# Kernel optimization log

Hardware: AMD Instinct MI355X
Metric: run time of the kernel (lower is better)

Reference implementation:

```python
import jax, jax.numpy as jnp
import numpy as np

B, C, S, HID = 64, 512, 28, 256  # batch, channels, spatial size, LSTM hidden


def _param(k, shape):
    return jax.random.normal(k, shape, jnp.float32) * 0.05


def setup_inputs() -> dict:
    key = jax.random.key(0)
    ks = jax.random.split(key, 19)
    inp = {"x": jax.random.normal(ks[0], (B, C, S, S), jnp.float32)}
    # vertical bidirectional LSTM (input C, hidden HID), torch gate order i,f,g,o
    inp["v_wih_f"] = _param(ks[1], (4 * HID, C))
    inp["v_whh_f"] = _param(ks[2], (4 * HID, HID))
    inp["v_b_f"] = _param(ks[3], (4 * HID,))
    inp["v_wih_b"] = _param(ks[4], (4 * HID, C))
    inp["v_whh_b"] = _param(ks[5], (4 * HID, HID))
    inp["v_b_b"] = _param(ks[6], (4 * HID,))
    # horizontal bidirectional LSTM (input 2*HID=512, hidden HID)
    inp["h_wih_f"] = _param(ks[7], (4 * HID, 2 * HID))
    inp["h_whh_f"] = _param(ks[8], (4 * HID, HID))
    inp["h_b_f"] = _param(ks[9], (4 * HID,))
    inp["h_wih_b"] = _param(ks[10], (4 * HID, 2 * HID))
    inp["h_whh_b"] = _param(ks[11], (4 * HID, HID))
    inp["h_b_b"] = _param(ks[12], (4 * HID,))
    # 1x1 conv 512 -> 100 (10x10 attention kernel logits)
    inp["conv_w"] = _param(ks[13], (100, 2 * HID))
    inp["conv_b"] = _param(ks[14], (100,))
    return inp


def _lstm_scan(xs, wih, whh, b):
    # xs: [T, N, D] -> h sequence [T, N, HID]
    hdim = whh.shape[1]
    def step(carry, xt):
        h, c = carry
        gates = xt @ wih.T + h @ whh.T + b  # [N, 4H]
        i, f, g, o = jnp.split(gates, 4, axis=-1)
        c = jax.nn.sigmoid(f) * c + jax.nn.sigmoid(i) * jnp.tanh(g)
        h = jax.nn.sigmoid(o) * jnp.tanh(c)
        return (h, c), h
    n = xs.shape[1]
    z = jnp.zeros((n, hdim), xs.dtype)
    _, hs = jax.lax.scan(step, (z, z), xs)
    return hs


def _bilstm(x, wf, uf, bf, wb, ub, bb):
    # x: [N, T, D] -> [N, T, 2*HID]
    xs = jnp.swapaxes(x, 0, 1)
    hf = _lstm_scan(xs, wf, uf, bf)
    hb = _lstm_scan(xs[::-1], wb, ub, bb)[::-1]
    return jnp.swapaxes(jnp.concatenate([hf, hb], axis=-1), 0, 1)


def reference(x, v_wih_f, v_whh_f, v_b_f, v_wih_b, v_whh_b, v_b_b,
              h_wih_f, h_whh_f, h_b_f, h_wih_b, h_whh_b, h_b_b,
              conv_w, conv_b):
    b, c, s, _ = x.shape
    xt = jnp.transpose(x, (0, 3, 2, 1))            # [B, W, H, C]
    # vertical LSTM: seq over W, batched over (B, H)
    v_in = jnp.transpose(xt, (0, 2, 1, 3)).reshape(b * s, s, c)
    v_out = _bilstm(v_in, v_wih_f, v_whh_f, v_b_f, v_wih_b, v_whh_b, v_b_b)
    v_out = jnp.transpose(v_out.reshape(b, s, s, 2 * HID), (0, 2, 1, 3))  # [B, W, H, 512]
    # horizontal LSTM: seq over H, batched over (B, W)
    h_in = v_out.reshape(b * s, s, 2 * HID)
    h_out = _bilstm(h_in, h_wih_f, h_whh_f, h_b_f, h_wih_b, h_whh_b, h_b_b)
    feat = jnp.transpose(h_out.reshape(b, s, s, 2 * HID), (0, 3, 2, 1))  # [B, 512, H, W]
    # 1x1 conv -> [B, 100, H, W], softmax over 100 kernel entries
    kern = jnp.einsum('bfhw,of->bohw', feat, conv_w) + conv_b[None, :, None, None]
    kern = jax.nn.softmax(kern, axis=1)
    # faithful to torch: C-order reshape [B,100,H,W] -> (B*H*W, 100) kernels
    w = kern.reshape(b, s * s, 100)
    # grouped dilated conv3d == weighted sum over dilation-3 sampled 10x10 grid
    x_s = x[:, :, ::3, ::3].reshape(b, c, 100)     # [B, C, 100]
    out = jnp.einsum('bpk,bck->bpc', w, x_s)       # [B, H*W, C]
    return out.reshape(b, c, s, s)                 # faithful C-order reshape
```

## Files before the change

### kernel.cpp

```cpp
#include <hip/hip_runtime.h>
#include <hip/hip_bf16.h>
#include <stdint.h>

typedef __hip_bfloat16 bf16_t;
typedef __attribute__((ext_vector_type(8))) short short8;
typedef __attribute__((ext_vector_type(4))) short short4v;
typedef __attribute__((ext_vector_type(4))) float f32x4;
typedef __attribute__((ext_vector_type(4))) unsigned int u32x4;
typedef unsigned long long ull;

#define MFMA16(a, b, c) __builtin_amdgcn_mfma_f32_16x16x32_bf16(a, b, c, 0, 0, 0)

#define NROW 50176
#define NBATCH 1792

__device__ __forceinline__ void g2l16(const void* g, void* l) {
  __builtin_amdgcn_global_load_lds(
      (const __attribute__((address_space(1))) unsigned int*)g,
      (__attribute__((address_space(3))) unsigned int*)l, 16, 0, 0);
}
__device__ __forceinline__ float sigm(float x) { return 1.0f / (1.0f + __expf(-x)); }
__device__ __forceinline__ float tanh_(float x) { return 2.0f / (1.0f + __expf(-2.0f * x)) - 1.0f; }
__device__ __forceinline__ void stc(bf16_t* p, float v) { *p = __float2bfloat16(v); }
__device__ __forceinline__ void stc(float* p, float v) { *p = v; }
__device__ __forceinline__ float bf2f(unsigned short u) {
  return __uint_as_float((unsigned int)u << 16);
}

struct CvtArgs {
  const float* src[8];
  bf16_t* dst[8];
  int n[8];
};
__global__ void cvt_all(CvtArgs a) {
  int arr = blockIdx.y;
  int i = blockIdx.x * 256 + threadIdx.x;
  if (i < a.n[arr]) a.dst[arr][i] = __float2bfloat16(a.src[arr][i]);
}

__global__ void transpose_x(const float* __restrict__ x, bf16_t* __restrict__ Xin) {
  int c0 = blockIdx.x * 128, h = blockIdx.y, b = blockIdx.z;
  __shared__ __align__(16) short tile[128 * 29];
  const float* xb = x + ((size_t)b * 512 + c0) * 784 + h * 28;
  for (int e = threadIdx.x; e < 128 * 28; e += 256) {
    int cc = e / 28, w = e - cc * 28;
    tile[cc * 29 + w] = __bfloat16_as_short(__float2bfloat16(xb[(size_t)cc * 784 + w]));
  }
  __syncthreads();
  size_t orow0 = (size_t)(b * 28 + h) * 28;
  short* os = (short*)Xin;
  for (int e = threadIdx.x; e < 28 * 128; e += 256) {
    int w = e >> 7, cc = e & 127;
    int c = c0 + cc;
    os[(size_t)(c >> 5) * NROW * 32 + (orow0 + w) * 32 + (c & 31)] = tile[cc * 29 + w];
  }
}

__global__ void build_xs(const float* __restrict__ x, bf16_t* __restrict__ xs) {
  int c = blockIdx.x, b = blockIdx.y;
  int k = threadIdx.x;
  const float* xr = x + ((size_t)b * 512 + c) * 784;
  float v = 0.0f;
  if (k < 100) { int kh = k / 10, kw = k - kh * 10; v = xr[kh * 84 + kw * 3]; }
  xs[((size_t)b * 512 + c) * 128 + k] = __float2bfloat16(v);
}

__global__ void pad_conv(const float* __restrict__ cw, const float* __restrict__ cb,
                         bf16_t* __restrict__ cwp, float* __restrict__ cbp,
                         unsigned int* __restrict__ bar) {
  int r = blockIdx.x;
  if (r == 0)
    for (int i = threadIdx.x; i < 1792; i += 128) bar[i] = 0;
  for (int i = threadIdx.x; i < 512; i += 128)
    cwp[r * 512 + i] = __float2bfloat16((r < 100) ? cw[r * 512 + i] : 0.0f);
  if (r == 0) cbp[threadIdx.x] = (threadIdx.x < 100) ? cb[threadIdx.x] : 0.0f;
}

template <typename CT, bool CPERM>
__global__ __launch_bounds__(256) void gemm_bt(
    const bf16_t* __restrict__ A, const bf16_t* __restrict__ B0,
    const bf16_t* __restrict__ B1, const float* __restrict__ bias0,
    const float* __restrict__ bias1, CT* __restrict__ C, int M, int N, int K) {
  __shared__ __align__(16) short As[128 * 32];
  __shared__ __align__(16) short Bs[128 * 32];
  int tid = threadIdx.x;
  int nb = blockIdx.x;
  int bm0 = blockIdx.y * 128, bn0 = nb * 128;
  int lrow = tid >> 2, lseg = tid & 3;
  const char* Ag = (const char*)A + ((size_t)(bm0 + lrow) * 32 + lseg * 8) * 2;
  size_t Aadv = (size_t)M * 64;
  const float* biasp;
  const char *Bg1, *Bg2;
  int js = 0;
  if (CPERM) {
    int dir = nb >> 3;
    js = nb & 7;
    const bf16_t* Bsel = dir ? B1 : B0;
    biasp = dir ? bias1 : bias0;
    int br1 = (lrow & 3) * 256 + js * 32 + (lrow >> 2);
    int br2 = br1 + 16;
    Bg1 = (const char*)(Bsel + (size_t)br1 * K) + lseg * 16;
    Bg2 = (const char*)(Bsel + (size_t)br2 * K) + lseg * 16;
  } else {
    biasp = bias0 + bn0;
    Bg1 = (const char*)(B0 + (size_t)(bn0 + lrow) * K) + lseg * 16;
    Bg2 = Bg1 + (size_t)64 * K * 2;
  }
  int w = tid >> 6, l = tid & 63, lm = l & 15, lq = l >> 4;
  int wm = w & 1, wn = w >> 1;
  f32x4 acc[4][4] = {};
  for (int k0 = 0; k0 < K; k0 += 32) {
    g2l16(Ag, (char*)As + tid * 16);
    g2l16(Ag + 4096, (char*)As + 4096 + tid * 16);
    g2l16(Bg1, (char*)Bs + tid * 16);
    g2l16(Bg2, (char*)Bs + 4096 + tid * 16);
    Ag += Aadv; Bg1 += 64; Bg2 += 64;
    __syncthreads();
    short8 afr[4], bfr[4];
#pragma unroll
    for (int i = 0; i < 4; i++) {
      afr[i] = *(const short8*)&As[(wm * 64 + i * 16 + lm) * 32 + lq * 8];
      bfr[i] = *(const short8*)&Bs[(wn * 64 + i * 16 + lm) * 32 + lq * 8];
    }
#pragma unroll
    for (int mi = 0; mi < 4; mi++)
#pragma unroll
      for (int ni = 0; ni < 4; ni++) acc[mi][ni] = MFMA16(afr[mi], bfr[ni], acc[mi][ni]);
    __syncthreads();
  }
  float bv[4];
#pragma unroll
  for (int ni = 0; ni < 4; ni++) {
    int cb = wn * 64 + ni * 16 + lm;
    bv[ni] = CPERM ? biasp[(cb & 3) * 256 + js * 32 + (cb >> 2)] : biasp[cb];
  }
#pragma unroll
  for (int mi = 0; mi < 4; mi++)
#pragma unroll
    for (int ni = 0; ni < 4; ni++) {
      int col = bn0 + wn * 64 + ni * 16 + lm;
#pragma unroll
      for (int r = 0; r < 4; r++) {
        size_t row = bm0 + wm * 64 + mi * 16 + lq * 4 + r;
        stc(&C[row * N + col], acc[mi][ni][r] + bv[ni]);
      }
    }
}

__global__ __launch_bounds__(256, 2) void lstm_scan(
    const bf16_t* __restrict__ G, const bf16_t* __restrict__ whh_f,
    const bf16_t* __restrict__ whh_b, bf16_t* __restrict__ hA,
    bf16_t* __restrict__ hB, bf16_t* __restrict__ outb,
    unsigned int* __restrict__ bar) {
  int dir = blockIdx.y;
  int js = blockIdx.x & 7;
  int rg = blockIdx.x >> 3;
  int tid = threadIdx.x, w = tid >> 6, l = tid & 63, lm = l & 15, lq = l >> 4;
  const short* whh = (const short*)(dir ? whh_b : whh_f);
  __shared__ __align__(16) short Ws[128 * 256];
  __shared__ __align__(16) short ht[64 * 40];
#pragma unroll
  for (int i = 0; i < 16; i++) {
    int segid = i * 256 + tid;
    int row = segid >> 5, seg = segid & 31;
    int gate = row >> 5, jj = row & 31;
    short8 v = *(const short8*)&whh[((size_t)(gate * 256 + js * 32 + jj)) * 256 + seg * 8];
    *(short8*)&Ws[row * 256 + ((seg ^ (row & 7)) * 8)] = v;
  }
  __syncthreads();
  unsigned int* cnt = bar + (dir * 28 + rg) * 16;
  int r0 = rg * 64 + w * 16;
  size_t dbase = (size_t)dir * 458752;

  const unsigned short* gb[2][4];
#pragma unroll
  for (int nj = 0; nj < 2; nj++)
#pragma unroll
    for (int r = 0; r < 4; r++) {
      int bi = r0 + lq * 4 + r;
      gb[nj][r] = (const unsigned short*)G + (size_t)bi * 28 * 2048 + (size_t)dir * 1024 +
                  js * 128 + (nj * 16 + lm) * 4;
    }
  size_t hro = (dbase + (size_t)(r0 + lm) * 32 + lq * 8) >> 2;
  int srow = tid >> 2, sseg = tid & 3;
  int sbi = rg * 64 + srow;
  size_t hwo = (dbase + (size_t)js * 57344 + (size_t)sbi * 32 + sseg * 8) >> 2;
  int sbb = sbi / 28, srr = sbi - sbb * 28;
  short* obase = (short*)outb + (size_t)(dir * 8 + js) * NROW * 32 +
                 ((size_t)sbb * 784 + srr) * 32 + sseg * 8;

  float creg[2][4] = {};
  ull gq[2][4], gqn[2][4];
  {
    size_t tofs = (size_t)(dir ? 27 : 0) * 2048;
#pragma unroll
    for (int nj = 0; nj < 2; nj++)
#pragma unroll
      for (int r = 0; r < 4; r++) gq[nj][r] = *(const ull*)(gb[nj][r] + tofs);
  }
#pragma unroll 1
  for (int s = 0; s < 28; s++) {
    int t = dir ? 27 - s : s;
    f32x4 acc[4][2] = {};
    if (s > 0) {
      const ull* hrp = (const ull*)((s & 1) ? hA : hB);
      ull hq[8][2];
#pragma unroll
      for (int kk = 0; kk < 8; kk++) {
        size_t o = hro + (size_t)kk * 14336;
        hq[kk][0] = __hip_atomic_load(hrp + o, __ATOMIC_RELAXED, __HIP_MEMORY_SCOPE_AGENT);
        hq[kk][1] =
            __hip_atomic_load(hrp + o + 1, __ATOMIC_RELAXED, __HIP_MEMORY_SCOPE_AGENT);
      }
      if (s < 27) {
        size_t tofs = (size_t)(dir ? 26 - s : s + 1) * 2048;
#pragma unroll
        for (int nj = 0; nj < 2; nj++)
#pragma unroll
          for (int r = 0; r < 4; r++) gqn[nj][r] = *(const ull*)(gb[nj][r] + tofs);
      }
#pragma unroll
      for (int kk = 0; kk < 8; kk++) {
        short8 a;
        ((ull*)&a)[0] = hq[kk][0];
        ((ull*)&a)[1] = hq[kk][1];
        int bseg = ((kk * 4 + lq) ^ (lm & 7)) * 8;
#pragma unroll
        for (int gate = 0; gate < 4; gate++)
#pragma unroll
          for (int nj = 0; nj < 2; nj++) {
            short8 b = *(const short8*)&Ws[(gate * 32 + nj * 16 + lm) * 256 + bseg];
            acc[gate][nj] = MFMA16(a, b, acc[gate][nj]);
          }
      }
    } else {
      size_t tofs = (size_t)(dir ? 26 : 1) * 2048;
#pragma unroll
      for (int nj = 0; nj < 2; nj++)
#pragma unroll
        for (int r = 0; r < 4; r++) gqn[nj][r] = *(const ull*)(gb[nj][r] + tofs);
    }
#pragma unroll
    for (int nj = 0; nj < 2; nj++)
#pragma unroll
      for (int r = 0; r < 4; r++) {
        short4v g4 = *(short4v*)&gq[nj][r];
        float gi = bf2f((unsigned short)g4[0]) + acc[0][nj][r];
        float gf = bf2f((unsigned short)g4[1]) + acc[1][nj][r];
        float gg = bf2f((unsigned short)g4[2]) + acc[2][nj][r];
        float go = bf2f((unsigned short)g4[3]) + acc[3][nj][r];
        float cn = sigm(gf) * creg[nj][r] + sigm(gi) * tanh_(gg);
        float hn = sigm(go) * tanh_(cn);
        creg[nj][r] = cn;
        ht[(w * 16 + lq * 4 + r) * 40 + nj * 16 + lm] =
            __bfloat16_as_short(__float2bfloat16(hn));
      }
    __syncthreads();
    {
      u32x4 v = *(const u32x4*)&ht[srow * 40 + sseg * 8];
      ull* hwp = (ull*)((s & 1) ? hB : hA);
      ull q0 = ((const ull*)&v)[0];
      ull q1 = ((const ull*)&v)[1];
      __hip_atomic_store(hwp + hwo, q0, __ATOMIC_RELAXED, __HIP_MEMORY_SCOPE_AGENT);
      __hip_atomic_store(hwp + hwo + 1, q1, __ATOMIC_RELAXED, __HIP_MEMORY_SCOPE_AGENT);
      *(u32x4*)(obase + (size_t)t * 896) = v;
    }
    if (s < 27) {
      asm volatile("s_waitcnt vmcnt(0)" ::: "memory");
      __syncthreads();
      if (tid == 0) {
        __hip_atomic_fetch_add(cnt, 1u, __ATOMIC_RELAXED, __HIP_MEMORY_SCOPE_AGENT);
        unsigned int tgt = 8u * (unsigned)(s + 1);
        while (__hip_atomic_load(cnt, __ATOMIC_RELAXED, __HIP_MEMORY_SCOPE_AGENT) < tgt)
          __builtin_amdgcn_s_sleep(2);
      }
      __syncthreads();
      __builtin_amdgcn_sched_barrier(0);
#pragma unroll
      for (int nj = 0; nj < 2; nj++)
#pragma unroll
        for (int r = 0; r < 4; r++) gq[nj][r] = gqn[nj][r];
    }
  }
}

__global__ void softmax_scatter(const float* __restrict__ P, bf16_t* __restrict__ Wscr) {
  int row = blockIdx.x;
  int l = threadIdx.x;
  int b = row / 784, q = row - b * 784;
  const float* pr = P + (size_t)row * 128;
  float v0 = (l < 100) ? pr[l] : -1e30f;
  float v1 = (l + 64 < 100) ? pr[l + 64] : -1e30f;
  float m = fmaxf(v0, v1);
  for (int off = 32; off > 0; off >>= 1) m = fmaxf(m, __shfl_down(m, off));
  m = __shfl(m, 0);
  float e0 = (l < 100) ? __expf(v0 - m) : 0.0f;
  float e1 = (l + 64 < 100) ? __expf(v1 - m) : 0.0f;
  float sum = e0 + e1;
  for (int off = 32; off > 0; off >>= 1) sum += __shfl_down(sum, off);
  sum = __shfl(sum, 0);
  float inv = 1.0f / sum;
  size_t base = (size_t)b * 784 * 128;
  if (l < 100) {
    int mm = l * 784 + q;
    Wscr[base + (size_t)(mm / 100) * 128 + (mm % 100)] = __float2bfloat16(e0 * inv);
  }
  int o = l + 64;
  if (o < 100) {
    int mm = o * 784 + q;
    Wscr[base + (size_t)(mm / 100) * 128 + (mm % 100)] = __float2bfloat16(e1 * inv);
  }
}

__global__ __launch_bounds__(256) void final_gemm(const bf16_t* __restrict__ Wscr,
                                                  const bf16_t* __restrict__ xs,
                                                  float* __restrict__ outp) {
  int m0 = blockIdx.x * 112, n0 = blockIdx.y * 128, b = blockIdx.z;
  int tid = threadIdx.x, w = tid >> 6, l = tid & 63, lm = l & 15, lq = l >> 4;
  const short* Ab = (const short*)Wscr + (size_t)b * 784 * 128;
  const short* Bb = (const short*)xs + (size_t)b * 512 * 128;
  f32x4 acc[7][2] = {};
#pragma unroll
  for (int kk = 0; kk < 4; kk++) {
    short8 b0 = *(const short8*)&Bb[(size_t)(n0 + w * 32 + lm) * 128 + kk * 32 + lq * 8];
    short8 b1 = *(const short8*)&Bb[(size_t)(n0 + w * 32 + 16 + lm) * 128 + kk * 32 + lq * 8];
#pragma unroll
    for (int mi = 0; mi < 7; mi++) {
      short8 a = *(const short8*)&Ab[(size_t)(m0 + mi * 16 + lm) * 128 + kk * 32 + lq * 8];
      acc[mi][0] = MFMA16(a, b0, acc[mi][0]);
      acc[mi][1] = MFMA16(a, b1, acc[mi][1]);
    }
  }
#pragma unroll
  for (int mi = 0; mi < 7; mi++)
#pragma unroll
    for (int ni = 0; ni < 2; ni++) {
      int c = n0 + w * 32 + ni * 16 + lm;
#pragma unroll
      for (int r = 0; r < 4; r++) {
        int p = m0 + mi * 16 + lq * 4 + r;
        outp[(size_t)b * 401408 + (size_t)p * 512 + c] = acc[mi][ni][r];
      }
    }
}

extern "C" void kernel_launch(void* const* d_in, const int* in_sizes, int n_in,
                              void* d_out, int out_size, void* d_ws, size_t ws_size,
                              hipStream_t stream) {
  const float* x = (const float*)d_in[0];
  const float* v_wih_f = (const float*)d_in[1];
  const float* v_whh_f = (const float*)d_in[2];
  const float* v_b_f = (const float*)d_in[3];
  const float* v_wih_b = (const float*)d_in[4];
  const float* v_whh_b = (const float*)d_in[5];
  const float* v_b_b = (const float*)d_in[6];
  const float* h_wih_f = (const float*)d_in[7];
  const float* h_whh_f = (const float*)d_in[8];
  const float* h_b_f = (const float*)d_in[9];
  const float* h_wih_b = (const float*)d_in[10];
  const float* h_whh_b = (const float*)d_in[11];
  const float* h_b_b = (const float*)d_in[12];
  const float* conv_w = (const float*)d_in[13];
  const float* conv_b = (const float*)d_in[14];

  char* ws = (char*)d_ws;
  bf16_t* Xin = (bf16_t*)(ws);
  bf16_t* Vout = (bf16_t*)(ws + 51380224);
  bf16_t* G = (bf16_t*)(ws + 102760448);
  float* P = (float*)(ws + 102760448);
  bf16_t* Wscr = (bf16_t*)(ws + 128450560);
  bf16_t* xs = (bf16_t*)(ws + 308281344);
  bf16_t* cwp = (bf16_t*)(ws + 316669952);
  float* cbp = (float*)(ws + 316801024);
  bf16_t* hstate = (bf16_t*)(ws + 316801536);
  unsigned int* bar = (unsigned int*)(ws + 318636544);
  bf16_t* wvf = (bf16_t*)(ws + 322306560);
  bf16_t* wvb = (bf16_t*)(ws + 323355136);
  bf16_t* uvf = (bf16_t*)(ws + 324403712);
  bf16_t* uvb = (bf16_t*)(ws + 324928000);
  bf16_t* whf = (bf16_t*)(ws + 325452288);
  bf16_t* whb = (bf16_t*)(ws + 326500864);
  bf16_t* uhf = (bf16_t*)(ws + 327549440);
  bf16_t* uhb = (bf16_t*)(ws + 328073728);
  bf16_t* Hout = Xin;

  CvtArgs ca;
  ca.src[0] = v_wih_f; ca.dst[0] = wvf; ca.n[0] = 524288;
  ca.src[1] = v_wih_b; ca.dst[1] = wvb; ca.n[1] = 524288;
  ca.src[2] = v_whh_f; ca.dst[2] = uvf; ca.n[2] = 262144;
  ca.src[3] = v_whh_b; ca.dst[3] = uvb; ca.n[3] = 262144;
  ca.src[4] = h_wih_f; ca.dst[4] = whf; ca.n[4] = 524288;
  ca.src[5] = h_wih_b; ca.dst[5] = whb; ca.n[5] = 524288;
  ca.src[6] = h_whh_f; ca.dst[6] = uhf; ca.n[6] = 262144;
  ca.src[7] = h_whh_b; ca.dst[7] = uhb; ca.n[7] = 262144;
  cvt_all<<<dim3(2048, 8), 256, 0, stream>>>(ca);

  transpose_x<<<dim3(4, 28, 64), 256, 0, stream>>>(x, Xin);
  build_xs<<<dim3(512, 64), 128, 0, stream>>>(x, xs);
  pad_conv<<<dim3(128), 128, 0, stream>>>(conv_w, conv_b, cwp, cbp, bar);

  gemm_bt<bf16_t, true><<<dim3(16, 392), 256, 0, stream>>>(
      Xin, wvf, wvb, v_b_f, v_b_b, G, NROW, 2048, 512);
  lstm_scan<<<dim3(224, 2), 256, 0, stream>>>(G, uvf, uvb, hstate, Xin, Vout, bar);

  gemm_bt<bf16_t, true><<<dim3(16, 392), 256, 0, stream>>>(
      Vout, whf, whb, h_b_f, h_b_b, G, NROW, 2048, 512);
  lstm_scan<<<dim3(224, 2), 256, 0, stream>>>(G, uhf, uhb, hstate, Vout, Hout, bar + 896);

  gemm_bt<float, false><<<dim3(1, 392), 256, 0, stream>>>(
      Hout, cwp, cwp, cbp, cbp, P, NROW, 128, 512);
  softmax_scatter<<<dim3(50176), 64, 0, stream>>>(P, Wscr);
  final_gemm<<<dim3(7, 4, 64), 256, 0, stream>>>(Wscr, xs, (float*)d_out);
}
```

Before: 1.054 ms.

## Interleave forward and backward LSTM directions in one block to hide barrier latency

```diff
diff --git a/kernel.cpp b/kernel.cpp
--- a/kernel.cpp
+++ b/kernel.cpp
@@ -13,6 +13,8 @@
 
 #define NROW 50176
 #define NBATCH 1792
+
+template <int N> struct IC { static constexpr int v = N; };
 
 __device__ __forceinline__ void g2l16(const void* g, void* l) {
   __builtin_amdgcn_global_load_lds(
@@ -147,30 +149,31 @@
     }
 }
 
-__global__ __launch_bounds__(256, 2) void lstm_scan(
+__global__ __launch_bounds__(256, 1) void lstm_scan(
     const bf16_t* __restrict__ G, const bf16_t* __restrict__ whh_f,
     const bf16_t* __restrict__ whh_b, bf16_t* __restrict__ hA,
     bf16_t* __restrict__ hB, bf16_t* __restrict__ outb,
     unsigned int* __restrict__ bar) {
-  int dir = blockIdx.y;
   int js = blockIdx.x & 7;
   int rg = blockIdx.x >> 3;
   int tid = threadIdx.x, w = tid >> 6, l = tid & 63, lm = l & 15, lq = l >> 4;
-  const short* whh = (const short*)(dir ? whh_b : whh_f);
-  __shared__ __align__(16) short Ws[128 * 256];
-  __shared__ __align__(16) short ht[64 * 40];
-#pragma unroll
-  for (int i = 0; i < 16; i++) {
-    int segid = i * 256 + tid;
-    int row = segid >> 5, seg = segid & 31;
-    int gate = row >> 5, jj = row & 31;
-    short8 v = *(const short8*)&whh[((size_t)(gate * 256 + js * 32 + jj)) * 256 + seg * 8];
-    *(short8*)&Ws[row * 256 + ((seg ^ (row & 7)) * 8)] = v;
+  __shared__ __align__(16) short Ws[2][128 * 256];
+  __shared__ __align__(16) short ht[2][64 * 40];
+#pragma unroll
+  for (int d = 0; d < 2; d++) {
+    const short* whh = (const short*)(d ? whh_b : whh_f);
+#pragma unroll
+    for (int i = 0; i < 16; i++) {
+      int segid = i * 256 + tid;
+      int row = segid >> 5, seg = segid & 31;
+      int gate = row >> 5, jj = row & 31;
+      short8 v = *(const short8*)&whh[((size_t)(gate * 256 + js * 32 + jj)) * 256 + seg * 8];
+      *(short8*)&Ws[d][row * 256 + ((seg ^ (row & 7)) * 8)] = v;
+    }
   }
   __syncthreads();
-  unsigned int* cnt = bar + (dir * 28 + rg) * 16;
   int r0 = rg * 64 + w * 16;
-  size_t dbase = (size_t)dir * 458752;
+  const size_t HD = 458752 >> 2;
 
   const unsigned short* gb[2][4];
 #pragma unroll
@@ -178,32 +181,40 @@
 #pragma unroll
     for (int r = 0; r < 4; r++) {
       int bi = r0 + lq * 4 + r;
-      gb[nj][r] = (const unsigned short*)G + (size_t)bi * 28 * 2048 + (size_t)dir * 1024 +
-                  js * 128 + (nj * 16 + lm) * 4;
-    }
-  size_t hro = (dbase + (size_t)(r0 + lm) * 32 + lq * 8) >> 2;
+      gb[nj][r] = (const unsigned short*)G + (size_t)bi * 28 * 2048 + js * 128 +
+                  (nj * 16 + lm) * 4;
+    }
+  size_t hro = ((size_t)(r0 + lm) * 32 + lq * 8) >> 2;
   int srow = tid >> 2, sseg = tid & 3;
   int sbi = rg * 64 + srow;
-  size_t hwo = (dbase + (size_t)js * 57344 + (size_t)sbi * 32 + sseg * 8) >> 2;
+  size_t hwo = ((size_t)js * 57344 + (size_t)sbi * 32 + sseg * 8) >> 2;
   int sbb = sbi / 28, srr = sbi - sbb * 28;
-  short* obase = (short*)outb + (size_t)(dir * 8 + js) * NROW * 32 +
-                 ((size_t)sbb * 784 + srr) * 32 + sseg * 8;
-
-  float creg[2][4] = {};
-  ull gq[2][4], gqn[2][4];
-  {
-    size_t tofs = (size_t)(dir ? 27 : 0) * 2048;
-#pragma unroll
-    for (int nj = 0; nj < 2; nj++)
-#pragma unroll
-      for (int r = 0; r < 4; r++) gq[nj][r] = *(const ull*)(gb[nj][r] + tofs);
-  }
-#pragma unroll 1
-  for (int s = 0; s < 28; s++) {
-    int t = dir ? 27 - s : s;
+  short* ob0 = (short*)outb + (size_t)js * NROW * 32 + ((size_t)sbb * 784 + srr) * 32 +
+               sseg * 8;
+
+  float creg[2][2][4] = {};
+  ull gq[2][2][4];
+#pragma unroll
+  for (int nj = 0; nj < 2; nj++)
+#pragma unroll
+    for (int r = 0; r < 4; r++) {
+      gq[0][nj][r] = *(const ull*)(gb[nj][r]);
+      gq[1][nj][r] = *(const ull*)(gb[nj][r] + 27 * 2048 + 1024);
+    }
+
+  auto phase = [&](auto DC, int s, int tcur, int tnext) {
+    constexpr int d = decltype(DC)::v;
+    unsigned int* cnt = bar + (rg * 2 + d) * 16;
+    bool notlast = (s < 27);
     f32x4 acc[4][2] = {};
     if (s > 0) {
-      const ull* hrp = (const ull*)((s & 1) ? hA : hB);
+      if (tid == 0) {
+        unsigned int tgt = 8u * (unsigned)s;
+        while (__hip_atomic_load(cnt, __ATOMIC_RELAXED, __HIP_MEMORY_SCOPE_AGENT) < tgt)
+          __builtin_amdgcn_s_sleep(2);
+      }
+      __syncthreads();
+      const ull* hrp = (const ull*)((s & 1) ? hA : hB) + (size_t)d * HD;
       ull hq[8][2];
 #pragma unroll
       for (int kk = 0; kk < 8; kk++) {
@@ -212,13 +223,6 @@
         hq[kk][1] =
             __hip_atomic_load(hrp + o + 1, __ATOMIC_RELAXED, __HIP_MEMORY_SCOPE_AGENT);
       }
-      if (s < 27) {
-        size_t tofs = (size_t)(dir ? 26 - s : s + 1) * 2048;
-#pragma unroll
-        for (int nj = 0; nj < 2; nj++)
-#pragma unroll
-          for (int r = 0; r < 4; r++) gqn[nj][r] = *(const ull*)(gb[nj][r] + tofs);
-      }
 #pragma unroll
       for (int kk = 0; kk < 8; kk++) {
         short8 a;
@@ -229,58 +233,52 @@
         for (int gate = 0; gate < 4; gate++)
 #pragma unroll
           for (int nj = 0; nj < 2; nj++) {
-            short8 b = *(const short8*)&Ws[(gate * 32 + nj * 16 + lm) * 256 + bseg];
+            short8 b = *(const short8*)&Ws[d][(gate * 32 + nj * 16 + lm) * 256 + bseg];
             acc[gate][nj] = MFMA16(a, b, acc[gate][nj]);
           }
       }
-    } else {
-      size_t tofs = (size_t)(dir ? 26 : 1) * 2048;
-#pragma unroll
-      for (int nj = 0; nj < 2; nj++)
-#pragma unroll
-        for (int r = 0; r < 4; r++) gqn[nj][r] = *(const ull*)(gb[nj][r] + tofs);
     }
 #pragma unroll
     for (int nj = 0; nj < 2; nj++)
 #pragma unroll
       for (int r = 0; r < 4; r++) {
-        short4v g4 = *(short4v*)&gq[nj][r];
+        short4v g4 = *(short4v*)&gq[d][nj][r];
         float gi = bf2f((unsigned short)g4[0]) + acc[0][nj][r];
         float gf = bf2f((unsigned short)g4[1]) + acc[1][nj][r];
         float gg = bf2f((unsigned short)g4[2]) + acc[2][nj][r];
         float go = bf2f((unsigned short)g4[3]) + acc[3][nj][r];
-        float cn = sigm(gf) * creg[nj][r] + sigm(gi) * tanh_(gg);
+        float cn = sigm(gf) * creg[d][nj][r] + sigm(gi) * tanh_(gg);
         float hn = sigm(go) * tanh_(cn);
-        creg[nj][r] = cn;
-        ht[(w * 16 + lq * 4 + r) * 40 + nj * 16 + lm] =
+        creg[d][nj][r] = cn;
+        ht[d][(w * 16 + lq * 4 + r) * 40 + nj * 16 + lm] =
             __bfloat16_as_short(__float2bfloat16(hn));
       }
     __syncthreads();
-    {
-      u32x4 v = *(const u32x4*)&ht[srow * 40 + sseg * 8];
-      ull* hwp = (ull*)((s & 1) ? hB : hA);
-      ull q0 = ((const ull*)&v)[0];
-      ull q1 = ((const ull*)&v)[1];
+    u32x4 v = *(const u32x4*)&ht[d][srow * 40 + sseg * 8];
+    ull q0 = ((const ull*)&v)[0], q1 = ((const ull*)&v)[1];
+    if (notlast) {
+      ull* hwp = (ull*)((s & 1) ? hB : hA) + (size_t)d * HD;
       __hip_atomic_store(hwp + hwo, q0, __ATOMIC_RELAXED, __HIP_MEMORY_SCOPE_AGENT);
       __hip_atomic_store(hwp + hwo + 1, q1, __ATOMIC_RELAXED, __HIP_MEMORY_SCOPE_AGENT);
-      *(u32x4*)(obase + (size_t)t * 896) = v;
-    }
-    if (s < 27) {
       asm volatile("s_waitcnt vmcnt(0)" ::: "memory");
       __syncthreads();
-      if (tid == 0) {
+      if (tid == 0)
         __hip_atomic_fetch_add(cnt, 1u, __ATOMIC_RELAXED, __HIP_MEMORY_SCOPE_AGENT);
-        unsigned int tgt = 8u * (unsigned)(s + 1);
-        while (__hip_atomic_load(cnt, __ATOMIC_RELAXED, __HIP_MEMORY_SCOPE_AGENT) < tgt)
-          __builtin_amdgcn_s_sleep(2);
-      }
-      __syncthreads();
-      __builtin_amdgcn_sched_barrier(0);
+    }
+    *(u32x4*)(ob0 + (size_t)d * 8 * NROW * 32 + (size_t)tcur * 896) = v;
+    if (notlast) {
+      size_t tofs = (size_t)tnext * 2048 + d * 1024;
 #pragma unroll
       for (int nj = 0; nj < 2; nj++)
 #pragma unroll
-        for (int r = 0; r < 4; r++) gq[nj][r] = gqn[nj][r];
-    }
+        for (int r = 0; r < 4; r++) gq[d][nj][r] = *(const ull*)(gb[nj][r] + tofs);
+    }
+  };
+
+#pragma unroll 1
+  for (int s = 0; s < 28; s++) {
+    phase(IC<0>{}, s, s, s + 1);
+    phase(IC<1>{}, s, 27 - s, 26 - s);
   }
 }
 
@@ -401,11 +399,11 @@
 
   gemm_bt<bf16_t, true><<<dim3(16, 392), 256, 0, stream>>>(
       Xin, wvf, wvb, v_b_f, v_b_b, G, NROW, 2048, 512);
-  lstm_scan<<<dim3(224, 2), 256, 0, stream>>>(G, uvf, uvb, hstate, Xin, Vout, bar);
+  lstm_scan<<<dim3(224), 256, 0, stream>>>(G, uvf, uvb, hstate, Xin, Vout, bar);
 
   gemm_bt<bf16_t, true><<<dim3(16, 392), 256, 0, stream>>>(
       Vout, whf, whb, h_b_f, h_b_b, G, NROW, 2048, 512);
-  lstm_scan<<<dim3(224, 2), 256, 0, stream>>>(G, uhf, uhb, hstate, Vout, Hout, bar + 896);
+  lstm_scan<<<dim3(224), 256, 0, stream>>>(G, uhf, uhb, hstate, Vout, Hout, bar + 896);
 
   gemm_bt<float, false><<<dim3(1, 392), 256, 0, stream>>>(
       Hout, cwp, cwp, cbp, cbp, P, NROW, 128, 512);
```

New measurement: 1.202 ms. 14.0% more time.
